# Performance work log

Measured on AMD Instinct MI355X. Metric: run time of the kernel, lower is better.

## Reference

```python
import jax, jax.numpy as jnp
import numpy as np

N_NODES = 50000
N_EDGES = 1600000
IN_CH, HID_CH, OUT_CH = 256, 128, 64


def setup_inputs() -> dict:
    key = jax.random.key(0)
    k1, k2, k3, k4 = jax.random.split(key, 4)
    x = jax.random.normal(k1, (N_NODES, IN_CH), dtype=jnp.float32)
    edge_index = jax.random.randint(k2, (2, N_EDGES), 0, N_NODES, dtype=jnp.int64)
    # Glorot-style init for weights, zero bias (as PyG GCNConv)
    W1 = jax.random.normal(k3, (IN_CH, HID_CH), dtype=jnp.float32) * (1.0 / np.sqrt(IN_CH))
    b1 = jnp.zeros((HID_CH,), dtype=jnp.float32)
    W2 = jax.random.normal(k4, (HID_CH, OUT_CH), dtype=jnp.float32) * (1.0 / np.sqrt(HID_CH))
    b2 = jnp.zeros((OUT_CH,), dtype=jnp.float32)
    return {"x": x, "edge_index": edge_index, "W1": W1, "b1": b1, "W2": W2, "b2": b2}


def _gcn_norm(edge_index, num_nodes):
    # PyG GCNConv default: add self-loops, symmetric normalization deg^-1/2 A deg^-1/2
    loop = jnp.arange(num_nodes, dtype=edge_index.dtype)
    src = jnp.concatenate([edge_index[0], loop])
    dst = jnp.concatenate([edge_index[1], loop])
    deg = jax.ops.segment_sum(jnp.ones_like(dst, dtype=jnp.float32), dst, num_segments=num_nodes)
    dinv = jnp.where(deg > 0, jax.lax.rsqrt(jnp.maximum(deg, 1.0)), 0.0)
    norm = dinv[src] * dinv[dst]  # [E + N]
    return src, dst, norm


def _gcn_conv(x, src, dst, norm, W, b, num_nodes):
    h = x @ W                              # [N, C_out] dense GEMM first (PyG order)
    msg = h[src] * norm[:, None]           # gather + scale, [E+N, C_out]
    out = jax.ops.segment_sum(msg, dst, num_segments=num_nodes)  # scatter-add
    return out + b


def reference(x, edge_index, W1, b1, W2, b2):
    n = x.shape[0]
    src, dst, norm = _gcn_norm(edge_index, n)
    h = _gcn_conv(x, src, dst, norm, W1, b1, n)
    h = jax.nn.relu(h)
    # F.dropout(training=self.training): eval mode -> identity
    h = _gcn_conv(h, src, dst, norm, W2, b2, n)
    return jax.nn.log_softmax(h, axis=1)
```

## Files before the change

kernel.cpp:

```cpp
#include <hip/hip_runtime.h>
#include <math.h>

#define NN 50000
#define NE 1600000
#define NBIN 391
#define BINW 128
#define STCAP 6144
#define OVFCAP 32768
#define NBLK 512
#define EPB 3125

__device__ __forceinline__ float blo(unsigned u) { return __uint_as_float(u << 16); }
__device__ __forceinline__ float bhi(unsigned u) { return __uint_as_float(u & 0xffff0000u); }
__device__ __forceinline__ unsigned bpack(float a, float b) {
    unsigned ua = __float_as_uint(a), ub = __float_as_uint(b);
    ua += 0x7fffu + ((ua >> 16) & 1u);
    ub += 0x7fffu + ((ub >> 16) & 1u);
    return (ua >> 16) | (ub & 0xffff0000u);
}

__device__ __forceinline__ int edge_get(const void* ei, int is64, long long i) {
    return is64 ? (int)((const long long*)ei)[i] : ((const int*)ei)[i];
}

__global__ void k_detect(const unsigned int* __restrict__ e, int* flag) {
    unsigned int v = e[2 * threadIdx.x + 1];
    unsigned long long m = __ballot(v != 0u);
    if (threadIdx.x == 0) *flag = (m == 0ull) ? 1 : 0;
}

__global__ __launch_bounds__(256) void k_bin(const void* __restrict__ ei,
                                             const int* __restrict__ flag,
                                             int* __restrict__ bincnt,
                                             unsigned* __restrict__ staged,
                                             int* __restrict__ ovfcnt,
                                             unsigned* __restrict__ ovf) {
    __shared__ unsigned lpk[EPB];
    __shared__ int lhist[NBIN], lbase[NBIN], lcur[NBIN];
    int is64 = *flag;
    int t = threadIdx.x;
    long long e0 = (long long)blockIdx.x * EPB;
    for (int i = t; i < NBIN; i += 256) { lhist[i] = 0; lcur[i] = 0; }
    __syncthreads();
    for (int j = t; j < EPB; j += 256) {
        int s = edge_get(ei, is64, e0 + j);
        int d = edge_get(ei, is64, (long long)NE + e0 + j);
        unsigned p = ((unsigned)d << 16) | (unsigned)s;
        lpk[j] = p;
        atomicAdd(&lhist[d >> 7], 1);
    }
    __syncthreads();
    for (int i = t; i < NBIN; i += 256)
        lbase[i] = (lhist[i] > 0) ? atomicAdd(&bincnt[i], lhist[i]) : 0;
    __syncthreads();
    for (int j = t; j < EPB; j += 256) {
        unsigned p = lpk[j];
        int bin = p >> 23;
        int pos = lbase[bin] + atomicAdd(&lcur[bin], 1);
        if (pos < STCAP) {
            staged[(long long)bin * STCAP + pos] = p;
        } else {
            int o = atomicAdd(ovfcnt, 1);
            if (o < OVFCAP) ovf[o] = p;
        }
    }
}

__global__ __launch_bounds__(512) void k_binscan(const int* __restrict__ bincnt,
                                                 int* __restrict__ binbase) {
    __shared__ int s[512];
    int t = threadIdx.x;
    int v = (t < NBIN) ? bincnt[t] : 0;
    s[t] = v;
    __syncthreads();
#pragma unroll
    for (int off = 1; off < 512; off <<= 1) {
        int u = (t >= off) ? s[t - off] : 0;
        __syncthreads();
        s[t] += u;
        __syncthreads();
    }
    if (t < NBIN) binbase[t] = s[t] - v;
}

__global__ __launch_bounds__(256) void k_csr(const unsigned* __restrict__ staged,
                                             const int* __restrict__ bincnt,
                                             const int* __restrict__ binbase,
                                             const int* __restrict__ ovfcnt,
                                             const unsigned* __restrict__ ovf,
                                             int* __restrict__ rowstart,
                                             int* __restrict__ cnt,
                                             float* __restrict__ dinv,
                                             int* __restrict__ csr) {
    __shared__ int lcnt[BINW], lpre[BINW], lcur[BINW];
    int b = blockIdx.x, t = threadIdx.x;
    int n = min(bincnt[b], STCAP);
    int novf = *ovfcnt;
    const unsigned* st = staged + (long long)b * STCAP;
    if (t < BINW) { lcnt[t] = 0; lcur[t] = 0; }
    __syncthreads();
    for (int j = t; j < n; j += 256) atomicAdd(&lcnt[(st[j] >> 16) & (BINW - 1)], 1);
    for (int j = t; j < novf; j += 256) {
        unsigned p = ovf[j];
        if ((int)(p >> 23) == b) atomicAdd(&lcnt[(p >> 16) & (BINW - 1)], 1);
    }
    __syncthreads();
    if (t < BINW) lpre[t] = lcnt[t];
    __syncthreads();
#pragma unroll
    for (int off = 1; off < BINW; off <<= 1) {
        int u = (t < BINW && t >= off) ? lpre[t - off] : 0;
        __syncthreads();
        if (t < BINW && t >= off) lpre[t] += u;
        __syncthreads();
    }
    int base = binbase[b];
    if (t < BINW) {
        int c = lcnt[t];
        int ex = lpre[t] - c;
        lpre[t] = ex;
        int node = b * BINW + t;
        if (node < NN) {
            rowstart[node] = base + ex;
            cnt[node] = c;
            dinv[node] = rsqrtf((float)c + 1.0f);
        }
    }
    __syncthreads();
    for (int j = t; j < n; j += 256) {
        unsigned p = st[j];
        int dloc = (p >> 16) & (BINW - 1);
        int pos = base + lpre[dloc] + atomicAdd(&lcur[dloc], 1);
        csr[pos] = (int)(p & 0xffffu);
    }
    for (int j = t; j < novf; j += 256) {
        unsigned p = ovf[j];
        if ((int)(p >> 23) == b) {
            int dloc = (p >> 16) & (BINW - 1);
            int pos = base + lpre[dloc] + atomicAdd(&lcur[dloc], 1);
            csr[pos] = (int)(p & 0xffffu);
        }
    }
}

template <int K, int CN, bool XBF>
__global__ __launch_bounds__(256) void k_gemm_scale(const void* __restrict__ Xv,
                                                    const float* __restrict__ W,
                                                    const float* __restrict__ dinv,
                                                    unsigned int* __restrict__ outb) {
    const int BM = 64, KT = 16, G = CN / 64;
    __shared__ float As[KT][BM + 4];
    __shared__ float Bs[KT][CN];
    int tid = threadIdx.x;
    int tx = tid & 15, ty = tid >> 4;
    int row0 = blockIdx.x * BM;
    float acc[4][G * 4];
#pragma unroll
    for (int a = 0; a < 4; a++)
#pragma unroll
        for (int b = 0; b < G * 4; b++) acc[a][b] = 0.f;

    for (int k0 = 0; k0 < K; k0 += KT) {
        if (XBF) {
            if (tid < 128) {
                int r = tid >> 1, kc = tid & 1, rr = row0 + r;
                uint4 v = {0, 0, 0, 0};
                if (rr < NN)
                    v = ((const uint4*)Xv)[((long long)rr * K + k0 + 8 * kc) >> 3];
                int kb = 8 * kc;
                As[kb + 0][r] = blo(v.x); As[kb + 1][r] = bhi(v.x);
                As[kb + 2][r] = blo(v.y); As[kb + 3][r] = bhi(v.y);
                As[kb + 4][r] = blo(v.z); As[kb + 5][r] = bhi(v.z);
                As[kb + 6][r] = blo(v.w); As[kb + 7][r] = bhi(v.w);
            }
        } else {
            int r = tid >> 2, kc = tid & 3, rr = row0 + r;
            float4 v = {0.f, 0.f, 0.f, 0.f};
            if (rr < NN)
                v = *(const float4*)((const float*)Xv + (long long)rr * K + k0 + 4 * kc);
            int kb = 4 * kc;
            As[kb + 0][r] = v.x; As[kb + 1][r] = v.y;
            As[kb + 2][r] = v.z; As[kb + 3][r] = v.w;
        }
#pragma unroll
        for (int j = 0; j < (KT * CN / 4) / 256; j++) {
            int q = tid + 256 * j;
            int kk = q / (CN / 4), c4 = q % (CN / 4);
            *(float4*)&Bs[kk][4 * c4] = *(const float4*)&W[(long long)(k0 + kk) * CN + 4 * c4];
        }
        __syncthreads();
#pragma unroll
        for (int kk = 0; kk < KT; kk++) {
            float4 av = *(const float4*)&As[kk][ty * 4];
            float am[4] = {av.x, av.y, av.z, av.w};
            float bm[G][4];
#pragma unroll
            for (int g = 0; g < G; g++) {
                float4 bv = *(const float4*)&Bs[kk][g * 64 + tx * 4];
                bm[g][0] = bv.x; bm[g][1] = bv.y; bm[g][2] = bv.z; bm[g][3] = bv.w;
            }
#pragma unroll
            for (int mi = 0; mi < 4; mi++)
#pragma unroll
                for (int g = 0; g < G; g++)
#pragma unroll
                    for (int ni = 0; ni < 4; ni++)
                        acc[mi][g * 4 + ni] = fmaf(am[mi], bm[g][ni], acc[mi][g * 4 + ni]);
        }
        __syncthreads();
    }
#pragma unroll
    for (int mi = 0; mi < 4; mi++) {
        int r = row0 + ty * 4 + mi;
        if (r < NN) {
            float s = dinv[r];
#pragma unroll
            for (int g = 0; g < G; g++) {
                uint2 u;
                u.x = bpack(s * acc[mi][g * 4 + 0], s * acc[mi][g * 4 + 1]);
                u.y = bpack(s * acc[mi][g * 4 + 2], s * acc[mi][g * 4 + 3]);
                long long elem = (long long)r * CN + g * 64 + tx * 4;
                *(uint2*)(outb + (elem >> 1)) = u;
            }
        }
    }
}

__global__ __launch_bounds__(256) void k_gather_relu(const uint4* __restrict__ h,
                                                     const int* __restrict__ csr,
                                                     const int* __restrict__ rowstart,
                                                     const int* __restrict__ cnt,
                                                     const float* __restrict__ dinv,
                                                     const float* __restrict__ bias,
                                                     uint4* __restrict__ out) {
    int tid = threadIdx.x;
    int node = blockIdx.x * 16 + (tid >> 4);
    int cl = tid & 15;
    if (node >= NN) return;
    int beg = rowstart[node], n = cnt[node];
    float acc[8];
    {
        uint4 v = h[(long long)node * 16 + cl];
        acc[0] = blo(v.x); acc[1] = bhi(v.x); acc[2] = blo(v.y); acc[3] = bhi(v.y);
        acc[4] = blo(v.z); acc[5] = bhi(v.z); acc[6] = blo(v.w); acc[7] = bhi(v.w);
    }
    int j = 0;
    for (; j + 3 < n; j += 4) {
        int a0 = csr[beg + j], a1 = csr[beg + j + 1];
        int a2 = csr[beg + j + 2], a3 = csr[beg + j + 3];
        uint4 v0 = h[(long long)a0 * 16 + cl], v1 = h[(long long)a1 * 16 + cl];
        uint4 v2 = h[(long long)a2 * 16 + cl], v3 = h[(long long)a3 * 16 + cl];
        acc[0] += blo(v0.x); acc[1] += bhi(v0.x); acc[2] += blo(v0.y); acc[3] += bhi(v0.y);
        acc[4] += blo(v0.z); acc[5] += bhi(v0.z); acc[6] += blo(v0.w); acc[7] += bhi(v0.w);
        acc[0] += blo(v1.x); acc[1] += bhi(v1.x); acc[2] += blo(v1.y); acc[3] += bhi(v1.y);
        acc[4] += blo(v1.z); acc[5] += bhi(v1.z); acc[6] += blo(v1.w); acc[7] += bhi(v1.w);
        acc[0] += blo(v2.x); acc[1] += bhi(v2.x); acc[2] += blo(v2.y); acc[3] += bhi(v2.y);
        acc[4] += blo(v2.z); acc[5] += bhi(v2.z); acc[6] += blo(v2.w); acc[7] += bhi(v2.w);
        acc[0] += blo(v3.x); acc[1] += bhi(v3.x); acc[2] += blo(v3.y); acc[3] += bhi(v3.y);
        acc[4] += blo(v3.z); acc[5] += bhi(v3.z); acc[6] += blo(v3.w); acc[7] += bhi(v3.w);
    }
    for (; j < n; j++) {
        uint4 v = h[(long long)csr[beg + j] * 16 + cl];
        acc[0] += blo(v.x); acc[1] += bhi(v.x); acc[2] += blo(v.y); acc[3] += bhi(v.y);
        acc[4] += blo(v.z); acc[5] += bhi(v.z); acc[6] += blo(v.w); acc[7] += bhi(v.w);
    }
    float d = dinv[node];
    float4 b0 = *(const float4*)&bias[cl * 8];
    float4 b1 = *(const float4*)&bias[cl * 8 + 4];
    float r0 = fmaxf(fmaf(d, acc[0], b0.x), 0.f), r1 = fmaxf(fmaf(d, acc[1], b0.y), 0.f);
    float r2 = fmaxf(fmaf(d, acc[2], b0.z), 0.f), r3 = fmaxf(fmaf(d, acc[3], b0.w), 0.f);
    float r4 = fmaxf(fmaf(d, acc[4], b1.x), 0.f), r5 = fmaxf(fmaf(d, acc[5], b1.y), 0.f);
    float r6 = fmaxf(fmaf(d, acc[6], b1.z), 0.f), r7 = fmaxf(fmaf(d, acc[7], b1.w), 0.f);
    uint4 o;
    o.x = bpack(r0, r1); o.y = bpack(r2, r3); o.z = bpack(r4, r5); o.w = bpack(r6, r7);
    out[(long long)node * 16 + cl] = o;
}

__global__ __launch_bounds__(256) void k_gather_lsm(const uint4* __restrict__ h,
                                                    const int* __restrict__ csr,
                                                    const int* __restrict__ rowstart,
                                                    const int* __restrict__ cnt,
                                                    const float* __restrict__ dinv,
                                                    const float* __restrict__ bias,
                                                    float* __restrict__ out) {
    int tid = threadIdx.x;
    int node = blockIdx.x * 32 + (tid >> 3);
    int cl = tid & 7;
    if (node >= NN) return;
    int beg = rowstart[node], n = cnt[node];
    float acc[8];
    {
        uint4 v = h[(long long)node * 8 + cl];
        acc[0] = blo(v.x); acc[1] = bhi(v.x); acc[2] = blo(v.y); acc[3] = bhi(v.y);
        acc[4] = blo(v.z); acc[5] = bhi(v.z); acc[6] = blo(v.w); acc[7] = bhi(v.w);
    }
    int j = 0;
    for (; j + 3 < n; j += 4) {
        int a0 = csr[beg + j], a1 = csr[beg + j + 1];
        int a2 = csr[beg + j + 2], a3 = csr[beg + j + 3];
        uint4 v0 = h[(long long)a0 * 8 + cl], v1 = h[(long long)a1 * 8 + cl];
        uint4 v2 = h[(long long)a2 * 8 + cl], v3 = h[(long long)a3 * 8 + cl];
        acc[0] += blo(v0.x); acc[1] += bhi(v0.x); acc[2] += blo(v0.y); acc[3] += bhi(v0.y);
        acc[4] += blo(v0.z); acc[5] += bhi(v0.z); acc[6] += blo(v0.w); acc[7] += bhi(v0.w);
        acc[0] += blo(v1.x); acc[1] += bhi(v1.x); acc[2] += blo(v1.y); acc[3] += bhi(v1.y);
        acc[4] += blo(v1.z); acc[5] += bhi(v1.z); acc[6] += blo(v1.w); acc[7] += bhi(v1.w);
        acc[0] += blo(v2.x); acc[1] += bhi(v2.x); acc[2] += blo(v2.y); acc[3] += bhi(v2.y);
        acc[4] += blo(v2.z); acc[5] += bhi(v2.z); acc[6] += blo(v2.w); acc[7] += bhi(v2.w);
        acc[0] += blo(v3.x); acc[1] += bhi(v3.x); acc[2] += blo(v3.y); acc[3] += bhi(v3.y);
        acc[4] += blo(v3.z); acc[5] += bhi(v3.z); acc[6] += blo(v3.w); acc[7] += bhi(v3.w);
    }
    for (; j < n; j++) {
        uint4 v = h[(long long)csr[beg + j] * 8 + cl];
        acc[0] += blo(v.x); acc[1] += bhi(v.x); acc[2] += blo(v.y); acc[3] += bhi(v.y);
        acc[4] += blo(v.z); acc[5] += bhi(v.z); acc[6] += blo(v.w); acc[7] += bhi(v.w);
    }
    float d = dinv[node];
    float4 b0 = *(const float4*)&bias[cl * 8];
    float4 b1 = *(const float4*)&bias[cl * 8 + 4];
    float t[8];
    t[0] = fmaf(d, acc[0], b0.x); t[1] = fmaf(d, acc[1], b0.y);
    t[2] = fmaf(d, acc[2], b0.z); t[3] = fmaf(d, acc[3], b0.w);
    t[4] = fmaf(d, acc[4], b1.x); t[5] = fmaf(d, acc[5], b1.y);
    t[6] = fmaf(d, acc[6], b1.z); t[7] = fmaf(d, acc[7], b1.w);
    float m = t[0];
#pragma unroll
    for (int i = 1; i < 8; i++) m = fmaxf(m, t[i]);
#pragma unroll
    for (int o = 1; o < 8; o <<= 1) m = fmaxf(m, __shfl_xor(m, o));
    float ex = 0.f;
#pragma unroll
    for (int i = 0; i < 8; i++) ex += __expf(t[i] - m);
#pragma unroll
    for (int o = 1; o < 8; o <<= 1) ex += __shfl_xor(ex, o);
    float l = logf(ex);
    float4 w0 = {t[0] - m - l, t[1] - m - l, t[2] - m - l, t[3] - m - l};
    float4 w1 = {t[4] - m - l, t[5] - m - l, t[6] - m - l, t[7] - m - l};
    *(float4*)&out[(long long)node * 64 + cl * 8] = w0;
    *(float4*)&out[(long long)node * 64 + cl * 8 + 4] = w1;
}

extern "C" void kernel_launch(void* const* d_in, const int* in_sizes, int n_in,
                              void* d_out, int out_size, void* d_ws, size_t ws_size,
                              hipStream_t stream) {
    const float* x  = (const float*)d_in[0];
    const void*  ei = d_in[1];
    const float* W1 = (const float*)d_in[2];
    const float* b1 = (const float*)d_in[3];
    const float* W2 = (const float*)d_in[4];
    const float* b2 = (const float*)d_in[5];
    float* out = (float*)d_out;

    char* ws = (char*)d_ws;
    float*    dinv     = (float*)   (ws + 0x000000);
    int*      flag     = (int*)     (ws + 0x040000);
    int*      cnt      = (int*)     (ws + 0x050000);
    int*      rowstart = (int*)     (ws + 0x090000);
    int*      bincnt   = (int*)     (ws + 0x0D0000);
    int*      ovfcnt   = (int*)     (ws + 0x0D0000 + NBIN * 4);
    int*      binbase  = (int*)     (ws + 0x0D2000);
    unsigned* ovf      = (unsigned*)(ws + 0x0E0000);
    int*      csr      = (int*)     (ws + 0x120000);
    unsigned* h1       = (unsigned*)(ws + 0x740000);
    unsigned* out1     = (unsigned*)(ws + 0x1400000);
    unsigned* staged   = (unsigned*)(ws + 0x1400000);

    k_detect<<<1, 64, 0, stream>>>((const unsigned int*)ei, flag);
    hipMemsetAsync(bincnt, 0, (size_t)(NBIN + 1) * 4, stream);
    k_bin<<<NBLK, 256, 0, stream>>>(ei, flag, bincnt, staged, ovfcnt, ovf);
    k_binscan<<<1, 512, 0, stream>>>(bincnt, binbase);
    k_csr<<<NBIN, 256, 0, stream>>>(staged, bincnt, binbase, ovfcnt, ovf,
                                    rowstart, cnt, dinv, csr);

    k_gemm_scale<256, 128, false><<<(NN + 63) / 64, 256, 0, stream>>>(x, W1, dinv, h1);
    k_gather_relu<<<(NN + 15) / 16, 256, 0, stream>>>((const uint4*)h1, csr, rowstart, cnt,
                                                      dinv, b1, (uint4*)out1);

    k_gemm_scale<128, 64, true><<<(NN + 63) / 64, 256, 0, stream>>>(out1, W2, dinv, h1);
    k_gather_lsm<<<(NN + 31) / 32, 256, 0, stream>>>((const uint4*)h1, csr, rowstart, cnt,
                                                     dinv, b2, out);
}
```

Before: 293.3 us.

## Replace FP32 SIMT GEMMs with bf16 MFMA kernels using transposed bf16 weights in LDS

Both dense projection kernels are rewritten to use the 16x16x32 bf16 MFMA instruction instead of scalar FMA tiling. Each block converts the full weight matrix to bf16 and stores it transposed in shared memory, and A fragments are loaded straight from global memory (converted from fp32 for layer 1). This is meant to cut the compute cost of the GEMMs. In exchange, layer-1 inputs and weights are rounded to bf16, every block re-converts the whole weight matrix, and the scaled outputs are written as scattered 16-bit stores.

```diff
diff --git a/kernel.cpp b/kernel.cpp
--- a/kernel.cpp
+++ b/kernel.cpp
@@ -10,6 +10,10 @@
 #define NBLK 512
 #define EPB 3125
 
+typedef __attribute__((ext_vector_type(8))) short bf16x8;
+typedef __attribute__((ext_vector_type(4))) float f32x4;
+union frag_u { unsigned u[4]; bf16x8 v; };
+
 __device__ __forceinline__ float blo(unsigned u) { return __uint_as_float(u << 16); }
 __device__ __forceinline__ float bhi(unsigned u) { return __uint_as_float(u & 0xffff0000u); }
 __device__ __forceinline__ unsigned bpack(float a, float b) {
@@ -17,6 +21,11 @@
     ua += 0x7fffu + ((ua >> 16) & 1u);
     ub += 0x7fffu + ((ub >> 16) & 1u);
     return (ua >> 16) | (ub & 0xffff0000u);
+}
+__device__ __forceinline__ unsigned short b16(float a) {
+    unsigned ua = __float_as_uint(a);
+    ua += 0x7fffu + ((ua >> 16) & 1u);
+    return (unsigned short)(ua >> 16);
 }
 
 __device__ __forceinline__ int edge_get(const void* ei, int is64, long long i) {
@@ -143,85 +152,94 @@
     }
 }
 
-template <int K, int CN, bool XBF>
-__global__ __launch_bounds__(256) void k_gemm_scale(const void* __restrict__ Xv,
-                                                    const float* __restrict__ W,
-                                                    const float* __restrict__ dinv,
-                                                    unsigned int* __restrict__ outb) {
-    const int BM = 64, KT = 16, G = CN / 64;
-    __shared__ float As[KT][BM + 4];
-    __shared__ float Bs[KT][CN];
+__global__ __launch_bounds__(256) void k_mm1(const float* __restrict__ X,
+                                             const float* __restrict__ W,
+                                             const float* __restrict__ dinv,
+                                             unsigned short* __restrict__ outh) {
+    __shared__ unsigned short Wt[128][264];
     int tid = threadIdx.x;
-    int tx = tid & 15, ty = tid >> 4;
-    int row0 = blockIdx.x * BM;
-    float acc[4][G * 4];
-#pragma unroll
-    for (int a = 0; a < 4; a++)
-#pragma unroll
-        for (int b = 0; b < G * 4; b++) acc[a][b] = 0.f;
-
-    for (int k0 = 0; k0 < K; k0 += KT) {
-        if (XBF) {
-            if (tid < 128) {
-                int r = tid >> 1, kc = tid & 1, rr = row0 + r;
-                uint4 v = {0, 0, 0, 0};
-                if (rr < NN)
-                    v = ((const uint4*)Xv)[((long long)rr * K + k0 + 8 * kc) >> 3];
-                int kb = 8 * kc;
-                As[kb + 0][r] = blo(v.x); As[kb + 1][r] = bhi(v.x);
-                As[kb + 2][r] = blo(v.y); As[kb + 3][r] = bhi(v.y);
-                As[kb + 4][r] = blo(v.z); As[kb + 5][r] = bhi(v.z);
-                As[kb + 6][r] = blo(v.w); As[kb + 7][r] = bhi(v.w);
-            }
-        } else {
-            int r = tid >> 2, kc = tid & 3, rr = row0 + r;
-            float4 v = {0.f, 0.f, 0.f, 0.f};
-            if (rr < NN)
-                v = *(const float4*)((const float*)Xv + (long long)rr * K + k0 + 4 * kc);
-            int kb = 4 * kc;
-            As[kb + 0][r] = v.x; As[kb + 1][r] = v.y;
-            As[kb + 2][r] = v.z; As[kb + 3][r] = v.w;
-        }
-#pragma unroll
-        for (int j = 0; j < (KT * CN / 4) / 256; j++) {
-            int q = tid + 256 * j;
-            int kk = q / (CN / 4), c4 = q % (CN / 4);
-            *(float4*)&Bs[kk][4 * c4] = *(const float4*)&W[(long long)(k0 + kk) * CN + 4 * c4];
-        }
-        __syncthreads();
-#pragma unroll
-        for (int kk = 0; kk < KT; kk++) {
-            float4 av = *(const float4*)&As[kk][ty * 4];
-            float am[4] = {av.x, av.y, av.z, av.w};
-            float bm[G][4];
-#pragma unroll
-            for (int g = 0; g < G; g++) {
-                float4 bv = *(const float4*)&Bs[kk][g * 64 + tx * 4];
-                bm[g][0] = bv.x; bm[g][1] = bv.y; bm[g][2] = bv.z; bm[g][3] = bv.w;
-            }
-#pragma unroll
-            for (int mi = 0; mi < 4; mi++)
-#pragma unroll
-                for (int g = 0; g < G; g++)
-#pragma unroll
-                    for (int ni = 0; ni < 4; ni++)
-                        acc[mi][g * 4 + ni] = fmaf(am[mi], bm[g][ni], acc[mi][g * 4 + ni]);
-        }
-        __syncthreads();
-    }
-#pragma unroll
-    for (int mi = 0; mi < 4; mi++) {
-        int r = row0 + ty * 4 + mi;
-        if (r < NN) {
-            float s = dinv[r];
-#pragma unroll
-            for (int g = 0; g < G; g++) {
-                uint2 u;
-                u.x = bpack(s * acc[mi][g * 4 + 0], s * acc[mi][g * 4 + 1]);
-                u.y = bpack(s * acc[mi][g * 4 + 2], s * acc[mi][g * 4 + 3]);
-                long long elem = (long long)r * CN + g * 64 + tx * 4;
-                *(uint2*)(outb + (elem >> 1)) = u;
-            }
+    for (int idx = tid; idx < 128 * 256; idx += 256) {
+        int col = idx & 127, k = idx >> 7;
+        Wt[col][k] = b16(W[k * 128 + col]);
+    }
+    __syncthreads();
+    int w = tid >> 6, l = tid & 63;
+    int lr = l & 15, kg = l >> 4;
+    int row = blockIdx.x * 64 + w * 16 + lr;
+    long long rowc = min(row, NN - 1);
+    f32x4 acc[8];
+#pragma unroll
+    for (int cf = 0; cf < 8; cf++) acc[cf] = {0.f, 0.f, 0.f, 0.f};
+#pragma unroll
+    for (int ks = 0; ks < 8; ks++) {
+        int k0 = ks * 32 + kg * 8;
+        const float4* p = (const float4*)(X + rowc * 256 + k0);
+        float4 v0 = p[0], v1 = p[1];
+        frag_u a;
+        a.u[0] = bpack(v0.x, v0.y); a.u[1] = bpack(v0.z, v0.w);
+        a.u[2] = bpack(v1.x, v1.y); a.u[3] = bpack(v1.z, v1.w);
+#pragma unroll
+        for (int cf = 0; cf < 8; cf++) {
+            uint4 bb = *(const uint4*)&Wt[cf * 16 + lr][k0];
+            frag_u b;
+            b.u[0] = bb.x; b.u[1] = bb.y; b.u[2] = bb.z; b.u[3] = bb.w;
+            acc[cf] = __builtin_amdgcn_mfma_f32_16x16x32_bf16(a.v, b.v, acc[cf], 0, 0, 0);
+        }
+    }
+    int orow0 = blockIdx.x * 64 + w * 16 + kg * 4;
+#pragma unroll
+    for (int r = 0; r < 4; r++) {
+        int orow = orow0 + r;
+        if (orow < NN) {
+            float s = dinv[orow];
+#pragma unroll
+            for (int cf = 0; cf < 8; cf++)
+                outh[(long long)orow * 128 + cf * 16 + lr] = b16(s * acc[cf][r]);
+        }
+    }
+}
+
+__global__ __launch_bounds__(256) void k_mm2(const unsigned short* __restrict__ Xh,
+                                             const float* __restrict__ W,
+                                             const float* __restrict__ dinv,
+                                             unsigned short* __restrict__ outh) {
+    __shared__ unsigned short Wt[64][136];
+    int tid = threadIdx.x;
+    for (int idx = tid; idx < 64 * 128; idx += 256) {
+        int col = idx & 63, k = idx >> 6;
+        Wt[col][k] = b16(W[k * 64 + col]);
+    }
+    __syncthreads();
+    int w = tid >> 6, l = tid & 63;
+    int lr = l & 15, kg = l >> 4;
+    int row = blockIdx.x * 64 + w * 16 + lr;
+    long long rowc = min(row, NN - 1);
+    f32x4 acc[4];
+#pragma unroll
+    for (int cf = 0; cf < 4; cf++) acc[cf] = {0.f, 0.f, 0.f, 0.f};
+#pragma unroll
+    for (int ks = 0; ks < 4; ks++) {
+        int k0 = ks * 32 + kg * 8;
+        uint4 av = *(const uint4*)(Xh + rowc * 128 + k0);
+        frag_u a;
+        a.u[0] = av.x; a.u[1] = av.y; a.u[2] = av.z; a.u[3] = av.w;
+#pragma unroll
+        for (int cf = 0; cf < 4; cf++) {
+            uint4 bb = *(const uint4*)&Wt[cf * 16 + lr][k0];
+            frag_u b;
+            b.u[0] = bb.x; b.u[1] = bb.y; b.u[2] = bb.z; b.u[3] = bb.w;
+            acc[cf] = __builtin_amdgcn_mfma_f32_16x16x32_bf16(a.v, b.v, acc[cf], 0, 0, 0);
+        }
+    }
+    int orow0 = blockIdx.x * 64 + w * 16 + kg * 4;
+#pragma unroll
+    for (int r = 0; r < 4; r++) {
+        int orow = orow0 + r;
+        if (orow < NN) {
+            float s = dinv[orow];
+#pragma unroll
+            for (int cf = 0; cf < 4; cf++)
+                outh[(long long)orow * 64 + cf * 16 + lr] = b16(s * acc[cf][r]);
         }
     }
 }
@@ -351,18 +369,18 @@
     float* out = (float*)d_out;
 
     char* ws = (char*)d_ws;
-    float*    dinv     = (float*)   (ws + 0x000000);
-    int*      flag     = (int*)     (ws + 0x040000);
-    int*      cnt      = (int*)     (ws + 0x050000);
-    int*      rowstart = (int*)     (ws + 0x090000);
-    int*      bincnt   = (int*)     (ws + 0x0D0000);
-    int*      ovfcnt   = (int*)     (ws + 0x0D0000 + NBIN * 4);
-    int*      binbase  = (int*)     (ws + 0x0D2000);
-    unsigned* ovf      = (unsigned*)(ws + 0x0E0000);
-    int*      csr      = (int*)     (ws + 0x120000);
-    unsigned* h1       = (unsigned*)(ws + 0x740000);
-    unsigned* out1     = (unsigned*)(ws + 0x1400000);
-    unsigned* staged   = (unsigned*)(ws + 0x1400000);
+    float*          dinv     = (float*)   (ws + 0x000000);
+    int*            flag     = (int*)     (ws + 0x040000);
+    int*            cnt      = (int*)     (ws + 0x050000);
+    int*            rowstart = (int*)     (ws + 0x090000);
+    int*            bincnt   = (int*)     (ws + 0x0D0000);
+    int*            ovfcnt   = (int*)     (ws + 0x0D0000 + NBIN * 4);
+    int*            binbase  = (int*)     (ws + 0x0D2000);
+    unsigned*       ovf      = (unsigned*)(ws + 0x0E0000);
+    int*            csr      = (int*)     (ws + 0x120000);
+    unsigned short* h1       = (unsigned short*)(ws + 0x740000);
+    unsigned short* out1     = (unsigned short*)(ws + 0x1400000);
+    unsigned*       staged   = (unsigned*)(ws + 0x1400000);
 
     k_detect<<<1, 64, 0, stream>>>((const unsigned int*)ei, flag);
     hipMemsetAsync(bincnt, 0, (size_t)(NBIN + 1) * 4, stream);
@@ -371,11 +389,11 @@
     k_csr<<<NBIN, 256, 0, stream>>>(staged, bincnt, binbase, ovfcnt, ovf,
                                     rowstart, cnt, dinv, csr);
 
-    k_gemm_scale<256, 128, false><<<(NN + 63) / 64, 256, 0, stream>>>(x, W1, dinv, h1);
+    k_mm1<<<(NN + 63) / 64, 256, 0, stream>>>(x, W1, dinv, h1);
     k_gather_relu<<<(NN + 15) / 16, 256, 0, stream>>>((const uint4*)h1, csr, rowstart, cnt,
                                                       dinv, b1, (uint4*)out1);
 
-    k_gemm_scale<128, 64, true><<<(NN + 63) / 64, 256, 0, stream>>>(out1, W2, dinv, h1);
+    k_mm2<<<(NN + 63) / 64, 256, 0, stream>>>(out1, W2, dinv, h1);
     k_gather_lsm<<<(NN + 31) / 32, 256, 0, stream>>>((const uint4*)h1, csr, rowstart, cnt,
                                                      dinv, b2, out);
 }
```

New measurement: 247.6 us. -15.6%, faster.
